# Optimization experiments

Measured on AMD Instinct MI355X. Metric: run time of the kernel, lower is better.

## Reference

```python
import jax, jax.numpy as jnp
from jax import lax
import numpy as np

EPS = 1e-5


def _conv2d(x, w, b=None, pad=1):
    out = lax.conv_general_dilated(x, w, (1, 1), [(pad, pad), (pad, pad)],
                                   dimension_numbers=("NCHW", "OIHW", "NCHW"))
    if b is not None:
        out = out + b[None, :, None, None]
    return out


def _bilinear(x, py, px):
    # x: [B,C,H,W]; py/px: [B,K2,H,W] float sampling coords. Zero outside bounds.
    B, C, H, W = x.shape
    y0 = jnp.floor(py)
    x0 = jnp.floor(px)
    y1, x1 = y0 + 1.0, x0 + 1.0
    wy1 = py - y0
    wy0 = 1.0 - wy1
    wx1 = px - x0
    wx0 = 1.0 - wx1
    xf = x.reshape(B, C, H * W)

    def gather(yi, xi):
        valid = ((yi >= 0) & (yi < H) & (xi >= 0) & (xi < W)).astype(x.dtype)
        yc = jnp.clip(yi, 0, H - 1).astype(jnp.int32)
        xc = jnp.clip(xi, 0, W - 1).astype(jnp.int32)
        idx = (yc * W + xc).reshape(B, -1)  # [B, K2*H*W]
        g = jnp.take_along_axis(xf, idx[:, None, :], axis=2)  # [B,C,K2*H*W]
        return g.reshape(B, C, *yi.shape[1:]) * valid[:, None]

    return (gather(y0, x0) * (wy0 * wx0)[:, None] + gather(y0, x1) * (wy0 * wx1)[:, None]
            + gather(y1, x0) * (wy1 * wx0)[:, None] + gather(y1, x1) * (wy1 * wx1)[:, None])


def _deform_conv(x, w_off, b_off, w_mod, b_mod, w_reg):
    # DCNv2: k=3, stride=1, pad=1, mask = 2*sigmoid(modulator)
    B, C, H, W = x.shape
    K = 3
    K2 = K * K
    offset = _conv2d(x, w_off, b_off)                   # [B, 2*K2, H, W]
    mask = 2.0 * jax.nn.sigmoid(_conv2d(x, w_mod, b_mod))  # [B, K2, H, W]
    off = offset.reshape(B, K2, 2, H, W)
    oy, ox = off[:, :, 0], off[:, :, 1]                 # [B,K2,H,W]
    ky = (jnp.arange(K2) // K).astype(x.dtype)[None, :, None, None]
    kx = (jnp.arange(K2) % K).astype(x.dtype)[None, :, None, None]
    gi = jnp.arange(H, dtype=x.dtype)[None, None, :, None]
    gj = jnp.arange(W, dtype=x.dtype)[None, None, None, :]
    py = gi - 1.0 + ky + oy
    px = gj - 1.0 + kx + ox
    v = _bilinear(x, py, px) * mask[:, None]            # [B,C,K2,H,W]
    Co = w_reg.shape[0]
    return jnp.einsum("bckhw,ock->bohw", v, w_reg.reshape(Co, -1, K2))


def _bn_relu(x, gamma, beta, mean, var):
    scale = gamma * lax.rsqrt(var + EPS)
    return jax.nn.relu(x * scale[None, :, None, None] + (beta - mean * scale)[None, :, None, None])


def _conv_transpose(x, w, stride=2, pad=1):
    # torch ConvTranspose2d weight layout [Cin, Cout, kH, kW]
    k = w.shape[2]
    wf = jnp.flip(w, (2, 3)).transpose(1, 0, 2, 3)  # -> OIHW
    p = k - 1 - pad
    return lax.conv_general_dilated(x, wf, (1, 1), [(p, p), (p, p)],
                                    lhs_dilation=(stride, stride),
                                    dimension_numbers=("NCHW", "OIHW", "NCHW"))


def setup_inputs() -> dict:
    key = jax.random.key(0)
    ks = jax.random.split(key, 16)
    C, Co = 256, 256
    x = jax.random.normal(ks[0], (8, C, 64, 64), jnp.float32)
    return {
        "x": x,
        "w_off": jax.random.normal(ks[1], (18, C, 3, 3), jnp.float32) * 0.01,
        "b_off": jax.random.normal(ks[2], (18,), jnp.float32) * 0.01,
        "w_mod": jax.random.normal(ks[3], (9, C, 3, 3), jnp.float32) * 0.01,
        "b_mod": jax.random.normal(ks[4], (9,), jnp.float32) * 0.01,
        "w_reg": jax.random.normal(ks[5], (Co, C, 3, 3), jnp.float32) * 0.02,
        "bn1_gamma": jnp.ones((Co,), jnp.float32),
        "bn1_beta": jnp.zeros((Co,), jnp.float32),
        "bn1_mean": jax.random.normal(ks[6], (Co,), jnp.float32) * 0.1,
        "bn1_var": jax.random.uniform(ks[7], (Co,), jnp.float32, 0.5, 1.5),
        "w_up": jax.random.normal(ks[8], (Co, Co, 4, 4), jnp.float32) * 0.02,
        "bn2_gamma": jnp.ones((Co,), jnp.float32),
        "bn2_beta": jnp.zeros((Co,), jnp.float32),
        "bn2_mean": jax.random.normal(ks[9], (Co,), jnp.float32) * 0.1,
        "bn2_var": jax.random.uniform(ks[10], (Co,), jnp.float32, 0.5, 1.5),
    }


def reference(x, w_off, b_off, w_mod, b_mod, w_reg,
              bn1_gamma, bn1_beta, bn1_mean, bn1_var,
              w_up, bn2_gamma, bn2_beta, bn2_mean, bn2_var):
    h = _deform_conv(x, w_off, b_off, w_mod, b_mod, w_reg)
    h = _bn_relu(h, bn1_gamma, bn1_beta, bn1_mean, bn1_var)
    h = _conv_transpose(h, w_up, stride=2, pad=1)
    h = _bn_relu(h, bn2_gamma, bn2_beta, bn2_mean, bn2_var)
    return h
```

## Files before the change

kernel.cpp:

```cpp
#include <hip/hip_runtime.h>
#include <math.h>

#define EPSV 1e-5f

typedef __attribute__((ext_vector_type(8)))  short short8_t;
typedef __attribute__((ext_vector_type(16))) float f32x16;

static __device__ __forceinline__ short f2bf(float f) {
    union { float f; unsigned u; } v; v.f = f;
    unsigned r = (v.u + 0x7FFFu + ((v.u >> 16) & 1u)) >> 16;
    return (short)r;
}
static __device__ __forceinline__ unsigned pack2bf(float a, float b) {
    return (unsigned)(unsigned short)f2bf(a) | ((unsigned)(unsigned short)f2bf(b) << 16);
}
static __device__ __forceinline__ float bflo(unsigned u) {
    union { unsigned u; float f; } t; t.u = u << 16; return t.f;
}
static __device__ __forceinline__ float bfhi(unsigned u) {
    union { unsigned u; float f; } t; t.u = u & 0xffff0000u; return t.f;
}

__global__ void prep_A2(const float* __restrict__ w_reg, short* __restrict__ A2) {
    int gid = blockIdx.x * 256 + threadIdx.x;
    int l  = gid & 63;
    int ot = (gid >> 6) & 7;
    int s  = gid >> 9;
    int o  = ot * 32 + (l & 31);
    int tap = s >> 4;
    int cb  = (s & 15) * 16 + (l >> 5) * 8;
    short* dst = A2 + (size_t)gid * 8;
#pragma unroll
    for (int j = 0; j < 8; ++j)
        dst[j] = f2bf(w_reg[(o * 256 + cb + j) * 9 + tap]);
}

__global__ void prep_A1(const float* __restrict__ w_off,
                        const float* __restrict__ w_mod, short* __restrict__ A1) {
    int gid = blockIdx.x * 256 + threadIdx.x;
    int l  = gid & 63;
    int s  = gid >> 6;
    int tap = s >> 4;
    int cq  = s & 15;
    int co  = l & 31;
    int cb  = cq * 16 + (l >> 5) * 8;
    short* dst = A1 + (size_t)gid * 8;
#pragma unroll
    for (int j = 0; j < 8; ++j) {
        int c = cb + j;
        float v = 0.f;
        if (co < 18)      v = w_off[(co * 256 + c) * 9 + tap];
        else if (co < 27) v = w_mod[((co - 18) * 256 + c) * 9 + tap];
        dst[j] = f2bf(v);
    }
}

__global__ void prep_Aup(const float* __restrict__ w_up, short* __restrict__ Aup) {
    int gid = blockIdx.x * 256 + threadIdx.x;
    int l  = gid & 63;
    int ot = (gid >> 6) & 7;
    int s  = (gid >> 9) & 63;
    int sx = (gid >> 15) & 1;
    int sy = (gid >> 16) & 1;
    int chunk = s >> 4;
    int tap = (s >> 2) & 3;
    int ch  = s & 3;
    int ty = tap >> 1, tx = tap & 1;
    int o  = ot * 32 + (l & 31);
    int cb = chunk * 64 + ch * 16 + (l >> 5) * 8;
    int ky = (1 - sy) + 2 * ty;
    int kx = (1 - sx) + 2 * tx;
    short* dst = Aup + (size_t)gid * 8;
#pragma unroll
    for (int j = 0; j < 8; ++j)
        dst[j] = f2bf(w_up[((cb + j) * 256 + o) * 16 + ky * 4 + kx]);
}

__global__ __launch_bounds__(256) void k0_nhwc(
    const float* __restrict__ x, unsigned short* __restrict__ xT) {
    __shared__ unsigned short t[64 * 65];
    int bx = blockIdx.x;
    int b   = bx & 7;
    int hwt = (bx >> 3) & 63;
    int ct  = bx >> 9;
    int tid = threadIdx.x;
    int g   = tid >> 6;
    int l   = tid & 63;
    const float* xb = x + ((size_t)b * 256 + ct * 64) * 4096 + hwt * 64;
#pragma unroll
    for (int i = 0; i < 16; ++i) {
        int c_l = g * 16 + i;
        t[c_l * 65 + l] = (unsigned short)f2bf(xb[(size_t)c_l * 4096 + l]);
    }
    __syncthreads();
    unsigned short* xo = xT + ((size_t)b * 4096 + hwt * 64) * 256 + ct * 64;
#pragma unroll
    for (int i = 0; i < 16; ++i) {
        int hw_l = g * 16 + i;
        xo[(size_t)hw_l * 256 + l] = t[l * 65 + hw_l];
    }
}

__global__ __launch_bounds__(256, 2) void k1_mfma(
    const unsigned short* __restrict__ xT, const short* __restrict__ A1,
    const float* __restrict__ b_off, const float* __restrict__ b_mod,
    float* __restrict__ offmask) {
    __shared__ short xs[3 * 66 * 72];
    __shared__ float red[4][32][64];

    int bx = blockIdx.x;
    int b  = bx & 7;
    int h  = bx >> 3;
    int tid  = threadIdx.x;
    int lane = tid & 63;
    int wv   = tid >> 6;
    int ln = lane & 31;
    int lh = lane >> 5;

    if (tid < 192) {
        int r    = tid >> 6;
        int rest = tid & 63;
        int colp = (rest >> 5) * 65;
        int cd   = rest & 31;
        ((unsigned*)xs)[((r * 66 + colp) * 72 >> 1) + cd] = 0;
    }

    f32x16 acc[2];
#pragma unroll
    for (int pt = 0; pt < 2; ++pt)
#pragma unroll
        for (int r = 0; r < 16; ++r) acc[pt][r] = 0.f;

    const unsigned short* xTb = xT + (size_t)b * 4096 * 256;

    for (int cc = 0; cc < 256; cc += 64) {
#pragma unroll
        for (int it = 0; it < 6; ++it) {
            int e   = tid + it * 256;
            int ch8 = e & 7;
            int col = (e >> 3) & 63;
            int r   = e >> 9;
            int row = h - 1 + r;
            bool v  = (row >= 0) & (row <= 63);
            short8_t val = {0,0,0,0,0,0,0,0};
            if (v) val = *(const short8_t*)(xTb + ((size_t)row * 64 + col) * 256 + cc + ch8 * 8);
            *(short8_t*)&xs[(r * 66 + col + 1) * 72 + ch8 * 8] = val;
        }
        __syncthreads();

#pragma unroll
        for (int tap = 0; tap < 9; ++tap) {
            int ky = tap / 3, kx = tap - 3 * (tap / 3);
            int s = tap * 16 + (cc >> 4) + wv;
            short8_t afr = *(const short8_t*)(A1 + ((size_t)s * 64 + lane) * 8);
            const short* bp = &xs[(ky * 66 + ln + kx) * 72 + wv * 16 + lh * 8];
            short8_t b0 = *(const short8_t*)bp;
            short8_t b1 = *(const short8_t*)(bp + 32 * 72);
            acc[0] = __builtin_amdgcn_mfma_f32_32x32x16_bf16(afr, b0, acc[0], 0, 0, 0);
            acc[1] = __builtin_amdgcn_mfma_f32_32x32x16_bf16(afr, b1, acc[1], 0, 0, 0);
        }
        __syncthreads();
    }

#pragma unroll
    for (int pt = 0; pt < 2; ++pt)
#pragma unroll
        for (int reg = 0; reg < 16; ++reg) {
            int row = (reg & 3) + 8 * (reg >> 2) + 4 * lh;
            red[wv][row][pt * 32 + ln] = acc[pt][reg];
        }
    __syncthreads();

    int pos = tid & 63;
    int cg  = tid >> 6;
#pragma unroll
    for (int i = 0; i < 7; ++i) {
        int co = 4 * i + cg;
        if (co < 27) {
            float sum = red[0][co][pos] + red[1][co][pos]
                      + red[2][co][pos] + red[3][co][pos];
            if (co < 18) {
                sum += b_off[co];
            } else {
                sum += b_mod[co - 18];
                sum = 2.f / (1.f + expf(-sum));
            }
            offmask[((size_t)(b * 27 + co) << 12) + (h << 6) + pos] = sum;
        }
    }
}

__global__ __launch_bounds__(512, 4) void k2_deform(
    const unsigned short* __restrict__ xT, const float* __restrict__ offmask,
    const short* __restrict__ A2,
    const float* __restrict__ g1, const float* __restrict__ be1,
    const float* __restrict__ mu1, const float* __restrict__ va1,
    unsigned short* __restrict__ h1) {
    __shared__ unsigned short lds_v[64 * 264];
    __shared__ int   sidx[9][64][4];
    __shared__ float swt [9][64][4];

    int bx = blockIdx.x;
    int b  = bx & 7;
    int h  = bx >> 3;
    int tid  = threadIdx.x;
    int lane = tid & 63;
    int wv   = tid >> 6;
    int ln = lane & 31;
    int lh = lane >> 5;

#pragma unroll
    for (int it = 0; it < 2; ++it) {
        int e = it * 512 + tid;
        if (e < 576) {
            int tap = e >> 6;
            int pos = e & 63;
            const float* om = offmask + ((size_t)b * 27 << 12) + (h << 6) + pos;
            float oy = om[(size_t)(2 * tap) << 12];
            float ox = om[(size_t)(2 * tap + 1) << 12];
            float m2 = om[(size_t)(18 + tap) << 12];
            int ky = tap / 3, kx = tap - 3 * (tap / 3);
            float py = (float)(h - 1 + ky) + oy;
            float px = (float)(pos - 1 + kx) + ox;
            float y0f = floorf(py), x0f = floorf(px);
            float wy1 = py - y0f, wy0 = 1.f - wy1;
            float wx1 = px - x0f, wx0 = 1.f - wx1;
            int y0 = (int)y0f, xq = (int)x0f;
            int y1 = y0 + 1, x1 = xq + 1;
            bool vy0 = (y0 >= 0) & (y0 < 64), vy1 = (y1 >= 0) & (y1 < 64);
            bool vx0 = (xq >= 0) & (xq < 64), vx1 = (x1 >= 0) & (x1 < 64);
            int y0c = min(max(y0, 0), 63), y1c = min(max(y1, 0), 63);
            int x0c = min(max(xq, 0), 63), x1c = min(max(x1, 0), 63);
            sidx[tap][pos][0] = y0c * 64 + x0c;  swt[tap][pos][0] = (vy0 && vx0) ? m2 * wy0 * wx0 : 0.f;
            sidx[tap][pos][1] = y0c * 64 + x1c;  swt[tap][pos][1] = (vy0 && vx1) ? m2 * wy0 * wx1 : 0.f;
            sidx[tap][pos][2] = y1c * 64 + x0c;  swt[tap][pos][2] = (vy1 && vx0) ? m2 * wy1 * wx0 : 0.f;
            sidx[tap][pos][3] = y1c * 64 + x1c;  swt[tap][pos][3] = (vy1 && vx1) ? m2 * wy1 * wx1 : 0.f;
        }
    }
    __syncthreads();

    f32x16 acc[2];
#pragma unroll
    for (int pt = 0; pt < 2; ++pt)
#pragma unroll
        for (int r = 0; r < 16; ++r) acc[pt][r] = 0.f;

    const unsigned* xTb = (const unsigned*)(xT + (size_t)b * 4096 * 256);

    for (int k = 0; k < 9; ++k) {
#pragma unroll
        for (int q = 0; q < 8; ++q) {
            int pos = wv * 8 + q;
            float a0 = 0.f, a1 = 0.f, a2 = 0.f, a3 = 0.f;
#pragma unroll
            for (int i = 0; i < 4; ++i) {
                int   idx = sidx[k][pos][i];
                float wt  = swt[k][pos][i];
                const unsigned* cp = xTb + ((size_t)idx << 7) + (lane << 1);
                unsigned u0 = cp[0], u1 = cp[1];
                a0 = fmaf(wt, bflo(u0), a0);
                a1 = fmaf(wt, bfhi(u0), a1);
                a2 = fmaf(wt, bflo(u1), a2);
                a3 = fmaf(wt, bfhi(u1), a3);
            }
            unsigned* dst = (unsigned*)&lds_v[pos * 264 + lane * 4];
            dst[0] = pack2bf(a0, a1);
            dst[1] = pack2bf(a2, a3);
        }
        __syncthreads();

#pragma unroll 4
        for (int sl = 0; sl < 16; ++sl) {
            int s = k * 16 + sl;
            short8_t afr = *(const short8_t*)(A2 + (((size_t)s * 8 + wv) * 64 + lane) * 8);
            short8_t b0 = *(const short8_t*)&lds_v[ln        * 264 + sl * 16 + lh * 8];
            short8_t b1 = *(const short8_t*)&lds_v[(32 + ln) * 264 + sl * 16 + lh * 8];
            acc[0] = __builtin_amdgcn_mfma_f32_32x32x16_bf16(afr, b0, acc[0], 0, 0, 0);
            acc[1] = __builtin_amdgcn_mfma_f32_32x32x16_bf16(afr, b1, acc[1], 0, 0, 0);
        }
        __syncthreads();
    }

#pragma unroll
    for (int reg = 0; reg < 16; ++reg) {
        int o = wv * 32 + (reg & 3) + 8 * (reg >> 2) + 4 * lh;
        float sc = g1[o] / sqrtf(va1[o] + EPSV);
        float sh = be1[o] - mu1[o] * sc;
        size_t ob = ((size_t)(b * 256 + o) * 64 + h) * 64;
#pragma unroll
        for (int pt = 0; pt < 2; ++pt) {
            float v = fmaxf(fmaf(acc[pt][reg], sc, sh), 0.f);
            h1[ob + pt * 32 + ln] = (unsigned short)f2bf(v);
        }
    }
}

__global__ __launch_bounds__(512, 2) void k3_convt(
    const unsigned short* __restrict__ h1, const short* __restrict__ Aup,
    const float* __restrict__ g2, const float* __restrict__ be2,
    const float* __restrict__ mu2, const float* __restrict__ va2,
    float* __restrict__ out) {
    __shared__ short lds[2 * 66 * 72];

    int bx = blockIdx.x;
    int b  = bx & 7;
    int y  = bx >> 3;
    int sy = y & 1;
    int m  = y >> 1;
    int tid  = threadIdx.x;
    int lane = tid & 63;
    int wv   = tid >> 6;
    int ow = wv & 3;
    int sx = wv >> 2;
    int ln = lane & 31;
    int lh = lane >> 5;

    int row0 = m + sy;
    int row1 = row0 - 1;
    bool v0 = (row0 <= 63);
    bool v1 = (row1 >= 0);

    if (tid < 288) {
        int r  = tid / 144;
        int rm = tid - r * 144;
        int cp = (rm / 72) * 65;
        int cc = rm - (rm / 72) * 72;
        lds[(r * 66 + cp) * 72 + cc] = 0;
    }

    f32x16 acc[2][2];
#pragma unroll
    for (int i = 0; i < 2; ++i)
#pragma unroll
        for (int mh = 0; mh < 2; ++mh)
#pragma unroll
            for (int r = 0; r < 16; ++r) acc[i][mh][r] = 0.f;

    const unsigned short* hb = h1 + (size_t)b * 256 * 4096;
    const short* Abase = Aup + (size_t)(sy * 2 + sx) * 64 * 8 * 64 * 8;
    int col = tid & 63;

    for (int cc = 0; cc < 256; cc += 64) {
#pragma unroll
        for (int it = 0; it < 4; ++it) {
            int quad = ((tid >> 6) & 7) + (it & 1) * 8;
            int r    = it >> 1;
            int row  = r ? row1 : row0;
            bool v   = r ? v1 : v0;
            int cb   = cc + quad * 4;
            unsigned short u0 = v ? hb[(size_t)(cb + 0) * 4096 + row * 64 + col] : 0;
            unsigned short u1 = v ? hb[(size_t)(cb + 1) * 4096 + row * 64 + col] : 0;
            unsigned short u2 = v ? hb[(size_t)(cb + 2) * 4096 + row * 64 + col] : 0;
            unsigned short u3 = v ? hb[(size_t)(cb + 3) * 4096 + row * 64 + col] : 0;
            unsigned* dst = (unsigned*)&lds[(r * 66 + col + 1) * 72 + quad * 4];
            dst[0] = (unsigned)u0 | ((unsigned)u1 << 16);
            dst[1] = (unsigned)u2 | ((unsigned)u3 << 16);
        }
        __syncthreads();

#pragma unroll
        for (int st = 0; st < 16; ++st) {
            int tap = st >> 2;
            int ch  = st & 3;
            int ty = tap >> 1, tx = tap & 1;
            int s_g = (cc >> 2) + st;
            const short* ap = Abase + (((size_t)s_g * 8) * 64 + lane) * 8;
            short8_t a0 = *(const short8_t*)(ap + (size_t)ow * 512);
            short8_t a1 = *(const short8_t*)(ap + (size_t)(ow + 4) * 512);
            int cbase = ty * 66 + ln + sx - tx + 1;
            short8_t b0 = *(const short8_t*)&lds[cbase * 72 + ch * 16 + lh * 8];
            short8_t b1 = *(const short8_t*)&lds[(cbase + 32) * 72 + ch * 16 + lh * 8];
            acc[0][0] = __builtin_amdgcn_mfma_f32_32x32x16_bf16(a0, b0, acc[0][0], 0, 0, 0);
            acc[0][1] = __builtin_amdgcn_mfma_f32_32x32x16_bf16(a0, b1, acc[0][1], 0, 0, 0);
            acc[1][0] = __builtin_amdgcn_mfma_f32_32x32x16_bf16(a1, b0, acc[1][0], 0, 0, 0);
            acc[1][1] = __builtin_amdgcn_mfma_f32_32x32x16_bf16(a1, b1, acc[1][1], 0, 0, 0);
        }
        __syncthreads();
    }

#pragma unroll
    for (int i = 0; i < 2; ++i) {
#pragma unroll
        for (int reg = 0; reg < 16; ++reg) {
            int o = (ow + 4 * i) * 32 + (reg & 3) + 8 * (reg >> 2) + 4 * lh;
            float sc = g2[o] / sqrtf(va2[o] + EPSV);
            float sh = be2[o] - mu2[o] * sc;
            size_t ob = ((size_t)(b * 256 + o) * 128 + y) * 128;
#pragma unroll
            for (int mh = 0; mh < 2; ++mh) {
                int x = 2 * (mh * 32 + ln) + sx;
                out[ob + x] = fmaxf(fmaf(acc[i][mh][reg], sc, sh), 0.f);
            }
        }
    }
}

extern "C" void kernel_launch(void* const* d_in, const int* in_sizes, int n_in,
                              void* d_out, int out_size, void* d_ws, size_t ws_size,
                              hipStream_t stream) {
    const float* x      = (const float*)d_in[0];
    const float* w_off  = (const float*)d_in[1];
    const float* b_off  = (const float*)d_in[2];
    const float* w_mod  = (const float*)d_in[3];
    const float* b_mod  = (const float*)d_in[4];
    const float* w_reg  = (const float*)d_in[5];
    const float* g1     = (const float*)d_in[6];
    const float* be1    = (const float*)d_in[7];
    const float* mu1    = (const float*)d_in[8];
    const float* va1    = (const float*)d_in[9];
    const float* w_up   = (const float*)d_in[10];
    const float* g2     = (const float*)d_in[11];
    const float* be2    = (const float*)d_in[12];
    const float* mu2    = (const float*)d_in[13];
    const float* va2    = (const float*)d_in[14];

    float* ws      = (float*)d_ws;
    float* offmask = ws;
    short* A2      = (short*)(offmask + 884736);
    short* A1      = A2 + 589824;
    short* Aup     = A1 + 73728;
    unsigned short* h1 = (unsigned short*)(Aup + 1048576);
    unsigned short* xT = h1 + 8388608;

    prep_A2   <<<288,  256, 0, stream>>>(w_reg, A2);
    prep_A1   <<<36,   256, 0, stream>>>(w_off, w_mod, A1);
    prep_Aup  <<<512,  256, 0, stream>>>(w_up, Aup);
    k0_nhwc   <<<2048, 256, 0, stream>>>(x, xT);
    k1_mfma   <<<512,  256, 0, stream>>>(xT, A1, b_off, b_mod, offmask);
    k2_deform <<<512,  512, 0, stream>>>(xT, offmask, A2, g1, be1, mu1, va1, h1);
    k3_convt  <<<1024, 512, 0, stream>>>(h1, Aup, g2, be2, mu2, va2, (float*)d_out);
}
```

Measured before the change: 381.8 us.

## Compute two output rows per block in transposed conv to reuse weights and input rows

The transposed-conv kernel now computes two output rows of the same parity per block, so it stages three input rows in shared memory instead of two. Each weight fragment is loaded once and reused for both rows, which cuts weight traffic and the number of redundant h1 row loads. The grid is halved to 512 blocks. In exchange, accumulator registers double (8 f32x16 tiles per wave), which may raise register pressure and reduce occupancy under launch_bounds(512,2).

```diff
diff --git a/kernel.cpp b/kernel.cpp
--- a/kernel.cpp
+++ b/kernel.cpp
@@ -300,13 +300,12 @@
     const float* __restrict__ g2, const float* __restrict__ be2,
     const float* __restrict__ mu2, const float* __restrict__ va2,
     float* __restrict__ out) {
-    __shared__ short lds[2 * 66 * 72];
+    __shared__ short lds[3 * 66 * 72];
 
     int bx = blockIdx.x;
     int b  = bx & 7;
-    int y  = bx >> 3;
-    int sy = y & 1;
-    int m  = y >> 1;
+    int sy = (bx >> 3) & 1;
+    int m0 = (bx >> 4) * 2;
     int tid  = threadIdx.x;
     int lane = tid & 63;
     int wv   = tid >> 6;
@@ -314,44 +313,43 @@
     int sx = wv >> 2;
     int ln = lane & 31;
     int lh = lane >> 5;
-
-    int row0 = m + sy;
-    int row1 = row0 - 1;
-    bool v0 = (row0 <= 63);
-    bool v1 = (row1 >= 0);
-
-    if (tid < 288) {
-        int r  = tid / 144;
-        int rm = tid - r * 144;
-        int cp = (rm / 72) * 65;
-        int cc = rm - (rm / 72) * 72;
-        lds[(r * 66 + cp) * 72 + cc] = 0;
-    }
-
-    f32x16 acc[2][2];
+    int col = lane;
+
+    int rbase = m0 + sy - 1;
+
+    if (tid < 192) {
+        int r    = tid >> 6;
+        int rest = tid & 63;
+        int colp = (rest >> 5) * 65;
+        int cd   = rest & 31;
+        ((unsigned*)lds)[((r * 66 + colp) * 72 >> 1) + cd] = 0;
+    }
+
+    f32x16 acc[2][2][2];
 #pragma unroll
     for (int i = 0; i < 2; ++i)
 #pragma unroll
-        for (int mh = 0; mh < 2; ++mh)
-#pragma unroll
-            for (int r = 0; r < 16; ++r) acc[i][mh][r] = 0.f;
+        for (int r = 0; r < 2; ++r)
+#pragma unroll
+            for (int mh = 0; mh < 2; ++mh)
+#pragma unroll
+                for (int e = 0; e < 16; ++e) acc[i][r][mh][e] = 0.f;
 
     const unsigned short* hb = h1 + (size_t)b * 256 * 4096;
-    const short* Abase = Aup + (size_t)(sy * 2 + sx) * 64 * 8 * 64 * 8;
-    int col = tid & 63;
+    const short* Abase = Aup + (size_t)(sy * 2 + sx) * 262144 + ow * 512 + lane * 8;
 
     for (int cc = 0; cc < 256; cc += 64) {
 #pragma unroll
-        for (int it = 0; it < 4; ++it) {
+        for (int it = 0; it < 6; ++it) {
             int quad = ((tid >> 6) & 7) + (it & 1) * 8;
             int r    = it >> 1;
-            int row  = r ? row1 : row0;
-            bool v   = r ? v1 : v0;
+            int row  = rbase + r;
+            bool v   = (row >= 0) & (row <= 63);
             int cb   = cc + quad * 4;
-            unsigned short u0 = v ? hb[(size_t)(cb + 0) * 4096 + row * 64 + col] : 0;
-            unsigned short u1 = v ? hb[(size_t)(cb + 1) * 4096 + row * 64 + col] : 0;
-            unsigned short u2 = v ? hb[(size_t)(cb + 2) * 4096 + row * 64 + col] : 0;
-            unsigned short u3 = v ? hb[(size_t)(cb + 3) * 4096 + row * 64 + col] : 0;
+            unsigned short u0 = v ? hb[(size_t)(cb + 0) * 4096 + row * 64 + col] : (unsigned short)0;
+            unsigned short u1 = v ? hb[(size_t)(cb + 1) * 4096 + row * 64 + col] : (unsigned short)0;
+            unsigned short u2 = v ? hb[(size_t)(cb + 2) * 4096 + row * 64 + col] : (unsigned short)0;
+            unsigned short u3 = v ? hb[(size_t)(cb + 3) * 4096 + row * 64 + col] : (unsigned short)0;
             unsigned* dst = (unsigned*)&lds[(r * 66 + col + 1) * 72 + quad * 4];
             dst[0] = (unsigned)u0 | ((unsigned)u1 << 16);
             dst[1] = (unsigned)u2 | ((unsigned)u3 << 16);
@@ -364,16 +362,18 @@
             int ch  = st & 3;
             int ty = tap >> 1, tx = tap & 1;
             int s_g = (cc >> 2) + st;
-            const short* ap = Abase + (((size_t)s_g * 8) * 64 + lane) * 8;
-            short8_t a0 = *(const short8_t*)(ap + (size_t)ow * 512);
-            short8_t a1 = *(const short8_t*)(ap + (size_t)(ow + 4) * 512);
-            int cbase = ty * 66 + ln + sx - tx + 1;
-            short8_t b0 = *(const short8_t*)&lds[cbase * 72 + ch * 16 + lh * 8];
-            short8_t b1 = *(const short8_t*)&lds[(cbase + 32) * 72 + ch * 16 + lh * 8];
-            acc[0][0] = __builtin_amdgcn_mfma_f32_32x32x16_bf16(a0, b0, acc[0][0], 0, 0, 0);
-            acc[0][1] = __builtin_amdgcn_mfma_f32_32x32x16_bf16(a0, b1, acc[0][1], 0, 0, 0);
-            acc[1][0] = __builtin_amdgcn_mfma_f32_32x32x16_bf16(a1, b0, acc[1][0], 0, 0, 0);
-            acc[1][1] = __builtin_amdgcn_mfma_f32_32x32x16_bf16(a1, b1, acc[1][1], 0, 0, 0);
+            short8_t a0 = *(const short8_t*)(Abase + (size_t)s_g * 4096);
+            short8_t a1 = *(const short8_t*)(Abase + (size_t)s_g * 4096 + 2048);
+#pragma unroll
+            for (int r = 0; r < 2; ++r) {
+                int cbase = (r + 1 - ty) * 66 + ln + sx - tx + 1;
+                short8_t b0 = *(const short8_t*)&lds[cbase * 72 + ch * 16 + lh * 8];
+                short8_t b1 = *(const short8_t*)&lds[(cbase + 32) * 72 + ch * 16 + lh * 8];
+                acc[0][r][0] = __builtin_amdgcn_mfma_f32_32x32x16_bf16(a0, b0, acc[0][r][0], 0, 0, 0);
+                acc[0][r][1] = __builtin_amdgcn_mfma_f32_32x32x16_bf16(a0, b1, acc[0][r][1], 0, 0, 0);
+                acc[1][r][0] = __builtin_amdgcn_mfma_f32_32x32x16_bf16(a1, b0, acc[1][r][0], 0, 0, 0);
+                acc[1][r][1] = __builtin_amdgcn_mfma_f32_32x32x16_bf16(a1, b1, acc[1][r][1], 0, 0, 0);
+            }
         }
         __syncthreads();
     }
@@ -385,11 +385,15 @@
             int o = (ow + 4 * i) * 32 + (reg & 3) + 8 * (reg >> 2) + 4 * lh;
             float sc = g2[o] / sqrtf(va2[o] + EPSV);
             float sh = be2[o] - mu2[o] * sc;
-            size_t ob = ((size_t)(b * 256 + o) * 128 + y) * 128;
-#pragma unroll
-            for (int mh = 0; mh < 2; ++mh) {
-                int x = 2 * (mh * 32 + ln) + sx;
-                out[ob + x] = fmaxf(fmaf(acc[i][mh][reg], sc, sh), 0.f);
+#pragma unroll
+            for (int r = 0; r < 2; ++r) {
+                int y = 2 * (m0 + r) + sy;
+                size_t ob = ((size_t)(b * 256 + o) * 128 + y) * 128;
+#pragma unroll
+                for (int mh = 0; mh < 2; ++mh) {
+                    int x = 2 * (mh * 32 + ln) + sx;
+                    out[ob + x] = fmaxf(fmaf(acc[i][r][mh][reg], sc, sh), 0.f);
+                }
             }
         }
     }
@@ -428,5 +432,5 @@
     k0_nhwc   <<<2048, 256, 0, stream>>>(x, xT);
     k1_mfma   <<<512,  256, 0, stream>>>(xT, A1, b_off, b_mod, offmask);
     k2_deform <<<512,  512, 0, stream>>>(xT, offmask, A2, g1, be1, mu1, va1, h1);
-    k3_convt  <<<1024, 512, 0, stream>>>(h1, Aup, g2, be2, mu2, va2, (float*)d_out);
-}
+    k3_convt  <<<512,  512, 0, stream>>>(h1, Aup, g2, be2, mu2, va2, (float*)d_out);
+}
```

After: 410.5 us. 7.5% more time.

## Double-buffer LDS and prefetch weights in transposed-conv MFMA loop

Applied to the files above, without the earlier changes.

The transposed-conv kernel now uses two LDS buffers. The next channel chunk is loaded from global into registers during compute and written to the alternate buffer, which leaves one barrier per chunk instead of two. Weight fragments are software-prefetched two steps ahead, MFMA sections run at raised wave priority, and launch bounds ask for 4 blocks per CU. The goal is to hide global-load latency behind the matrix work, at the cost of more registers and double the LDS, which may limit the occupancy the higher launch bound requests.

```diff
diff --git a/kernel.cpp b/kernel.cpp
--- a/kernel.cpp
+++ b/kernel.cpp
@@ -295,12 +295,12 @@
     }
 }
 
-__global__ __launch_bounds__(512, 2) void k3_convt(
+__global__ __launch_bounds__(512, 4) void k3_convt(
     const unsigned short* __restrict__ h1, const short* __restrict__ Aup,
     const float* __restrict__ g2, const float* __restrict__ be2,
     const float* __restrict__ mu2, const float* __restrict__ va2,
     float* __restrict__ out) {
-    __shared__ short lds[2 * 66 * 72];
+    __shared__ short lds[2][2 * 66 * 72];
 
     int bx = blockIdx.x;
     int b  = bx & 7;
@@ -314,6 +314,7 @@
     int sx = wv >> 2;
     int ln = lane & 31;
     int lh = lane >> 5;
+    int col = tid & 63;
 
     int row0 = m + sy;
     int row1 = row0 - 1;
@@ -324,8 +325,10 @@
         int r  = tid / 144;
         int rm = tid - r * 144;
         int cp = (rm / 72) * 65;
-        int cc = rm - (rm / 72) * 72;
-        lds[(r * 66 + cp) * 72 + cc] = 0;
+        int cz = rm - (rm / 72) * 72;
+#pragma unroll
+        for (int bi = 0; bi < 2; ++bi)
+            lds[bi][(r * 66 + cp) * 72 + cz] = 0;
     }
 
     f32x16 acc[2][2];
@@ -337,46 +340,82 @@
             for (int r = 0; r < 16; ++r) acc[i][mh][r] = 0.f;
 
     const unsigned short* hb = h1 + (size_t)b * 256 * 4096;
-    const short* Abase = Aup + (size_t)(sy * 2 + sx) * 64 * 8 * 64 * 8;
-    int col = tid & 63;
+    const short* Abase = Aup + (size_t)(sy * 2 + sx) * 262144 + ow * 512 + lane * 8;
+
+    unsigned short uS[4][4];
+
+#define LOADC(CC) {                                                          \
+    _Pragma("unroll")                                                        \
+    for (int it = 0; it < 4; ++it) {                                         \
+        int quad = ((tid >> 6) & 7) + (it & 1) * 8;                          \
+        int r    = it >> 1;                                                  \
+        int row  = r ? row1 : row0;                                          \
+        bool v   = r ? v1 : v0;                                              \
+        int cb   = (CC) + quad * 4;                                          \
+        const unsigned short* p = hb + (size_t)cb * 4096 + row * 64 + col;   \
+        uS[it][0] = v ? p[0]     : (unsigned short)0;                        \
+        uS[it][1] = v ? p[4096]  : (unsigned short)0;                        \
+        uS[it][2] = v ? p[8192]  : (unsigned short)0;                        \
+        uS[it][3] = v ? p[12288] : (unsigned short)0;                        \
+    } }
+
+#define WRITEC(L) {                                                         \
+    _Pragma("unroll")                                                       \
+    for (int it = 0; it < 4; ++it) {                                        \
+        int quad = ((tid >> 6) & 7) + (it & 1) * 8;                         \
+        int r    = it >> 1;                                                 \
+        unsigned* dst = (unsigned*)&(L)[(r * 66 + col + 1) * 72 + quad * 4];\
+        dst[0] = (unsigned)uS[it][0] | ((unsigned)uS[it][1] << 16);         \
+        dst[1] = (unsigned)uS[it][2] | ((unsigned)uS[it][3] << 16);         \
+    } }
+
+    LOADC(0);
+    WRITEC(lds[0]);
+    LOADC(64);
+    __syncthreads();
 
     for (int cc = 0; cc < 256; cc += 64) {
-#pragma unroll
-        for (int it = 0; it < 4; ++it) {
-            int quad = ((tid >> 6) & 7) + (it & 1) * 8;
-            int r    = it >> 1;
-            int row  = r ? row1 : row0;
-            bool v   = r ? v1 : v0;
-            int cb   = cc + quad * 4;
-            unsigned short u0 = v ? hb[(size_t)(cb + 0) * 4096 + row * 64 + col] : 0;
-            unsigned short u1 = v ? hb[(size_t)(cb + 1) * 4096 + row * 64 + col] : 0;
-            unsigned short u2 = v ? hb[(size_t)(cb + 2) * 4096 + row * 64 + col] : 0;
-            unsigned short u3 = v ? hb[(size_t)(cb + 3) * 4096 + row * 64 + col] : 0;
-            unsigned* dst = (unsigned*)&lds[(r * 66 + col + 1) * 72 + quad * 4];
-            dst[0] = (unsigned)u0 | ((unsigned)u1 << 16);
-            dst[1] = (unsigned)u2 | ((unsigned)u3 << 16);
-        }
-        __syncthreads();
-
+        int cur = (cc >> 6) & 1;
+        const short* L = lds[cur];
+
+        const short* Ac = Abase + (size_t)(cc >> 2) * 4096;
+        short8_t aA0 = *(const short8_t*)(Ac);
+        short8_t aA1 = *(const short8_t*)(Ac + 2048);
+        short8_t aB0 = *(const short8_t*)(Ac + 4096);
+        short8_t aB1 = *(const short8_t*)(Ac + 4096 + 2048);
+
+        __builtin_amdgcn_s_setprio(1);
 #pragma unroll
         for (int st = 0; st < 16; ++st) {
             int tap = st >> 2;
             int ch  = st & 3;
             int ty = tap >> 1, tx = tap & 1;
-            int s_g = (cc >> 2) + st;
-            const short* ap = Abase + (((size_t)s_g * 8) * 64 + lane) * 8;
-            short8_t a0 = *(const short8_t*)(ap + (size_t)ow * 512);
-            short8_t a1 = *(const short8_t*)(ap + (size_t)(ow + 4) * 512);
+            short8_t c0 = (st & 1) ? aB0 : aA0;
+            short8_t c1 = (st & 1) ? aB1 : aA1;
+            if (st < 14) {
+                const short* an = Ac + (size_t)(st + 2) * 4096;
+                if (st & 1) { aB0 = *(const short8_t*)an; aB1 = *(const short8_t*)(an + 2048); }
+                else        { aA0 = *(const short8_t*)an; aA1 = *(const short8_t*)(an + 2048); }
+            }
             int cbase = ty * 66 + ln + sx - tx + 1;
-            short8_t b0 = *(const short8_t*)&lds[cbase * 72 + ch * 16 + lh * 8];
-            short8_t b1 = *(const short8_t*)&lds[(cbase + 32) * 72 + ch * 16 + lh * 8];
-            acc[0][0] = __builtin_amdgcn_mfma_f32_32x32x16_bf16(a0, b0, acc[0][0], 0, 0, 0);
-            acc[0][1] = __builtin_amdgcn_mfma_f32_32x32x16_bf16(a0, b1, acc[0][1], 0, 0, 0);
-            acc[1][0] = __builtin_amdgcn_mfma_f32_32x32x16_bf16(a1, b0, acc[1][0], 0, 0, 0);
-            acc[1][1] = __builtin_amdgcn_mfma_f32_32x32x16_bf16(a1, b1, acc[1][1], 0, 0, 0);
-        }
-        __syncthreads();
-    }
+            short8_t b0 = *(const short8_t*)&L[cbase * 72 + ch * 16 + lh * 8];
+            short8_t b1 = *(const short8_t*)&L[(cbase + 32) * 72 + ch * 16 + lh * 8];
+            acc[0][0] = __builtin_amdgcn_mfma_f32_32x32x16_bf16(c0, b0, acc[0][0], 0, 0, 0);
+            acc[0][1] = __builtin_amdgcn_mfma_f32_32x32x16_bf16(c0, b1, acc[0][1], 0, 0, 0);
+            acc[1][0] = __builtin_amdgcn_mfma_f32_32x32x16_bf16(c1, b0, acc[1][0], 0, 0, 0);
+            acc[1][1] = __builtin_amdgcn_mfma_f32_32x32x16_bf16(c1, b1, acc[1][1], 0, 0, 0);
+        }
+        __builtin_amdgcn_s_setprio(0);
+
+        if (cc < 192) {
+            WRITEC(lds[cur ^ 1]);
+            if (cc < 128) LOADC(cc + 128);
+            __syncthreads();
+        }
+    }
+
+#undef LOADC
+#undef WRITEC
 
 #pragma unroll
     for (int i = 0; i < 2; ++i) {
```

Result: slower. 392.3 us (+2.7%).

## Store intermediate activation channel-last and stage full channel slab once in convT

Applied to the files above, without the earlier changes.

The deform-conv kernel now writes its bf16 output in position-major, channel-contiguous layout, staging through LDS to emit 16-byte vector stores instead of scattered 2-byte stores. The transposed-conv kernel then loads all 256 channels for both input rows into a larger LDS tile with 16-byte vector loads in one pass, removing the per-64-channel loop and its barriers. The cost is much more LDS per block (about 68 KB), which may reduce occupancy under the 2-blocks-per-CU launch bound, and the A-fragment index order changes to match.

```diff
diff --git a/kernel.cpp b/kernel.cpp
--- a/kernel.cpp
+++ b/kernel.cpp
@@ -282,16 +282,31 @@
     }
 
 #pragma unroll
-    for (int reg = 0; reg < 16; ++reg) {
-        int o = wv * 32 + (reg & 3) + 8 * (reg >> 2) + 4 * lh;
-        float sc = g1[o] / sqrtf(va1[o] + EPSV);
-        float sh = be1[o] - mu1[o] * sc;
-        size_t ob = ((size_t)(b * 256 + o) * 64 + h) * 64;
-#pragma unroll
-        for (int pt = 0; pt < 2; ++pt) {
-            float v = fmaxf(fmaf(acc[pt][reg], sc, sh), 0.f);
-            h1[ob + pt * 32 + ln] = (unsigned short)f2bf(v);
-        }
+    for (int pt = 0; pt < 2; ++pt) {
+        int pos = pt * 32 + ln;
+#pragma unroll
+        for (int rg = 0; rg < 4; ++rg) {
+            float v[4];
+#pragma unroll
+            for (int j = 0; j < 4; ++j) {
+                int o = wv * 32 + j + 8 * rg + 4 * lh;
+                float sc = g1[o] / sqrtf(va1[o] + EPSV);
+                float sh = be1[o] - mu1[o] * sc;
+                v[j] = fmaxf(fmaf(acc[pt][rg * 4 + j], sc, sh), 0.f);
+            }
+            unsigned* dst = (unsigned*)&lds_v[pos * 264 + wv * 32 + 8 * rg + 4 * lh];
+            dst[0] = pack2bf(v[0], v[1]);
+            dst[1] = pack2bf(v[2], v[3]);
+        }
+    }
+    __syncthreads();
+    {
+        int pos = tid >> 3;
+        int cb  = (tid & 7) * 32;
+        unsigned short* ho = h1 + ((size_t)(b * 64 + h) * 64 + pos) * 256 + cb;
+#pragma unroll
+        for (int kk = 0; kk < 4; ++kk)
+            *(short8_t*)&ho[kk * 8] = *(const short8_t*)&lds_v[pos * 264 + cb + kk * 8];
     }
 }
 
@@ -300,7 +315,7 @@
     const float* __restrict__ g2, const float* __restrict__ be2,
     const float* __restrict__ mu2, const float* __restrict__ va2,
     float* __restrict__ out) {
-    __shared__ short lds[2 * 66 * 72];
+    __shared__ short lds[2 * 66 * 260];
 
     int bx = blockIdx.x;
     int b  = bx & 7;
@@ -320,12 +335,25 @@
     bool v0 = (row0 <= 63);
     bool v1 = (row1 >= 0);
 
-    if (tid < 288) {
-        int r  = tid / 144;
-        int rm = tid - r * 144;
-        int cp = (rm / 72) * 65;
-        int cc = rm - (rm / 72) * 72;
-        lds[(r * 66 + cp) * 72 + cc] = 0;
+    {
+        int r  = tid >> 8;
+        int cp = ((tid >> 7) & 1) * 65;
+        int cd = tid & 127;
+        ((unsigned*)lds)[(((r * 66 + cp) * 260) >> 1) + cd] = 0;
+    }
+
+    const unsigned short* hb = h1 + (size_t)b * 4096 * 256;
+#pragma unroll
+    for (int it = 0; it < 8; ++it) {
+        int e   = tid + it * 512;
+        int c8  = e & 31;
+        int col = (e >> 5) & 63;
+        int r   = e >> 11;
+        int row = r ? row1 : row0;
+        bool v  = r ? v1 : v0;
+        short8_t val = {0,0,0,0,0,0,0,0};
+        if (v) val = *(const short8_t*)(hb + ((size_t)row * 64 + col) * 256 + c8 * 8);
+        *(short8_t*)&lds[(r * 66 + col + 1) * 260 + c8 * 8] = val;
     }
 
     f32x16 acc[2][2];
@@ -336,46 +364,28 @@
 #pragma unroll
             for (int r = 0; r < 16; ++r) acc[i][mh][r] = 0.f;
 
-    const unsigned short* hb = h1 + (size_t)b * 256 * 4096;
-    const short* Abase = Aup + (size_t)(sy * 2 + sx) * 64 * 8 * 64 * 8;
-    int col = tid & 63;
-
-    for (int cc = 0; cc < 256; cc += 64) {
-#pragma unroll
-        for (int it = 0; it < 4; ++it) {
-            int quad = ((tid >> 6) & 7) + (it & 1) * 8;
-            int r    = it >> 1;
-            int row  = r ? row1 : row0;
-            bool v   = r ? v1 : v0;
-            int cb   = cc + quad * 4;
-            unsigned short u0 = v ? hb[(size_t)(cb + 0) * 4096 + row * 64 + col] : 0;
-            unsigned short u1 = v ? hb[(size_t)(cb + 1) * 4096 + row * 64 + col] : 0;
-            unsigned short u2 = v ? hb[(size_t)(cb + 2) * 4096 + row * 64 + col] : 0;
-            unsigned short u3 = v ? hb[(size_t)(cb + 3) * 4096 + row * 64 + col] : 0;
-            unsigned* dst = (unsigned*)&lds[(r * 66 + col + 1) * 72 + quad * 4];
-            dst[0] = (unsigned)u0 | ((unsigned)u1 << 16);
-            dst[1] = (unsigned)u2 | ((unsigned)u3 << 16);
-        }
-        __syncthreads();
-
-#pragma unroll
-        for (int st = 0; st < 16; ++st) {
-            int tap = st >> 2;
-            int ch  = st & 3;
+    __syncthreads();
+
+    const short* Abase = Aup + (size_t)(sy * 2 + sx) * 262144 + ow * 512 + lane * 8;
+
+#pragma unroll 4
+    for (int cq = 0; cq < 16; ++cq) {
+#pragma unroll
+        for (int tap = 0; tap < 4; ++tap) {
+            int s_g = (cq >> 2) * 16 + tap * 4 + (cq & 3);
+            const short* ap = Abase + (size_t)s_g * 4096;
+            short8_t a0 = *(const short8_t*)(ap);
+            short8_t a1 = *(const short8_t*)(ap + 2048);
             int ty = tap >> 1, tx = tap & 1;
-            int s_g = (cc >> 2) + st;
-            const short* ap = Abase + (((size_t)s_g * 8) * 64 + lane) * 8;
-            short8_t a0 = *(const short8_t*)(ap + (size_t)ow * 512);
-            short8_t a1 = *(const short8_t*)(ap + (size_t)(ow + 4) * 512);
             int cbase = ty * 66 + ln + sx - tx + 1;
-            short8_t b0 = *(const short8_t*)&lds[cbase * 72 + ch * 16 + lh * 8];
-            short8_t b1 = *(const short8_t*)&lds[(cbase + 32) * 72 + ch * 16 + lh * 8];
+            const short* bp = &lds[cbase * 260 + cq * 16 + lh * 8];
+            short8_t b0 = *(const short8_t*)bp;
+            short8_t b1 = *(const short8_t*)(bp + 32 * 260);
             acc[0][0] = __builtin_amdgcn_mfma_f32_32x32x16_bf16(a0, b0, acc[0][0], 0, 0, 0);
             acc[0][1] = __builtin_amdgcn_mfma_f32_32x32x16_bf16(a0, b1, acc[0][1], 0, 0, 0);
             acc[1][0] = __builtin_amdgcn_mfma_f32_32x32x16_bf16(a1, b0, acc[1][0], 0, 0, 0);
             acc[1][1] = __builtin_amdgcn_mfma_f32_32x32x16_bf16(a1, b1, acc[1][1], 0, 0, 0);
         }
-        __syncthreads();
     }
 
 #pragma unroll
```

Result: slower. 430.7 us (+12.8%).
